# Optimization experiments

Measured on AMD Instinct MI355X. Metric: run time of the kernel, lower is better.

The kernel has to match this reference:

```python
import jax, jax.numpy as jnp
import numpy as np

N = 100000   # nodes
E = 1600000  # edges (self-loop free by construction)
B = 512      # graphs in batch
F = 128      # input node features
HID = 128    # hidden dim
HEADS = 4
CH = HID // HEADS  # 32
EPS_BN = 1e-5


def setup_inputs() -> dict:
    key = jax.random.key(0)
    ks = jax.random.split(key, 24)
    x = jax.random.normal(ks[0], (N, F), jnp.float32)
    dst = jax.random.randint(ks[1], (E,), 0, N)
    off = jax.random.randint(ks[2], (E,), 1, N)
    src = (dst + off) % N  # guaranteed no self loops
    edge_index = jnp.stack([src, dst]).astype(jnp.int32)
    batch = jnp.sort(jax.random.randint(ks[3], (N,), 0, B)).astype(jnp.int32)
    g = lambda k, shape, fan: jax.random.normal(k, shape, jnp.float32) / np.sqrt(fan)
    return {
        "x": x, "edge_index": edge_index, "batch": batch,
        "W_in": g(ks[4], (F, HID), F), "b_in": jnp.zeros((HID,), jnp.float32),
        "lin_w": g(ks[5], (2, HID, HID), HID),
        "att_src": g(ks[6], (2, HEADS, CH), CH),
        "att_dst": g(ks[7], (2, HEADS, CH), CH),
        "conv_b": jnp.zeros((2, HID), jnp.float32),
        "lin_w_last": g(ks[8], (HID, HID), HID),
        "att_src_last": g(ks[9], (HID,), HID),
        "att_dst_last": g(ks[10], (HID,), HID),
        "b_last": jnp.zeros((HID,), jnp.float32),
        "bn_g": jnp.ones((3, HID), jnp.float32) + 0.1 * jax.random.normal(ks[11], (3, HID), jnp.float32),
        "bn_b": 0.1 * jax.random.normal(ks[12], (3, HID), jnp.float32),
        "bn_m": 0.1 * jax.random.normal(ks[13], (3, HID), jnp.float32),
        "bn_v": 0.5 + jax.random.uniform(ks[14], (3, HID), jnp.float32),
        "ro_w1": g(ks[15], (HID, HID // 2), HID),
        "ro_b1": jnp.zeros((HID // 2,), jnp.float32),
        "ro_w2": g(ks[16], (HID // 2, 1), HID // 2),
        "ro_b2": jnp.zeros((1,), jnp.float32),
    }


def _gat_conv(h, src, dst, W, a_src, a_dst, bias, concat):
    """PyG GATConv (shared lin for src/dst, add_self_loops=True, eval mode)."""
    n = h.shape[0]
    heads, ch = a_src.shape
    xs = (h @ W).reshape(n, heads, ch)              # [N,H,C]
    al_s = jnp.sum(xs * a_src, axis=-1)             # [N,H]
    al_d = jnp.sum(xs * a_dst, axis=-1)             # [N,H]
    loop = jnp.arange(n, dtype=src.dtype)
    src_f = jnp.concatenate([src, loop])
    dst_f = jnp.concatenate([dst, loop])
    e = jax.nn.leaky_relu(al_s[src_f] + al_d[dst_f], 0.2)   # [E+N,H]
    m = jax.ops.segment_max(e, dst_f, num_segments=n)       # dest-grouped softmax
    ee = jnp.exp(e - m[dst_f])
    z = jax.ops.segment_sum(ee, dst_f, num_segments=n)
    alpha = ee / (z[dst_f] + 1e-16)                          # [E+N,H]
    out = jax.ops.segment_sum(alpha[:, :, None] * xs[src_f], dst_f, num_segments=n)
    out = out.reshape(n, heads * ch) if concat else jnp.mean(out, axis=1)
    return out + bias


def _bn_eval(h, g, b, m, v):
    return (h - m) * (g / jnp.sqrt(v + EPS_BN)) + b


def _seg_softmax(scores, seg, num_segments):
    m = jax.ops.segment_max(scores, seg, num_segments=num_segments)
    e = jnp.exp(scores - m[seg])
    z = jax.ops.segment_sum(e, seg, num_segments=num_segments)
    return e / z[seg]


def reference(x, edge_index, batch, W_in, b_in, lin_w, att_src, att_dst, conv_b,
              lin_w_last, att_src_last, att_dst_last, b_last,
              bn_g, bn_b, bn_m, bn_v, ro_w1, ro_b1, ro_w2, ro_b2):
    src, dst = edge_index[0], edge_index[1]
    h = x @ W_in + b_in                                       # input_proj
    # first num_layers-1 multi-head concat layers
    for i in range(2):
        h_new = _gat_conv(h, src, dst, lin_w[i], att_src[i], att_dst[i], conv_b[i], True)
        h_new = jax.nn.elu(_bn_eval(h_new, bn_g[i], bn_b[i], bn_m[i], bn_v[i]))
        h = h + h_new                                         # residual (shapes match)
    # final single-head layer, concat=False
    h_new = _gat_conv(h, src, dst, lin_w_last, att_src_last[None, :], att_dst_last[None, :], b_last, False)
    h_new = jax.nn.elu(_bn_eval(h_new, bn_g[2], bn_b[2], bn_m[2], bn_v[2]))
    h = h + h_new
    # attention readout + per-graph softmax over atoms
    atom_scores = (jnp.tanh(h @ ro_w1 + ro_b1) @ ro_w2 + ro_b2)[:, 0]   # [N]
    atom_attention = _seg_softmax(atom_scores, batch, B)
    # attention-weighted add pool
    graph_emb = jax.ops.segment_sum(h * atom_attention[:, None], batch, num_segments=B)
    return graph_emb, atom_attention
```

## Files before the change

kernel.cpp:

```cpp
#include <hip/hip_runtime.h>
#include <math.h>
#include <stdint.h>

#define BSZ 512
#define BSH 9
#define NBKT_MAX 256

typedef __attribute__((ext_vector_type(8))) short bf16x8;
typedef __attribute__((ext_vector_type(4))) float f32x4;

static __device__ __forceinline__ uint32_t f2bf(float x) {
    uint32_t u = __float_as_uint(x);
    return (u + 0x7fffu + ((u >> 16) & 1u)) >> 16;
}
static __device__ __forceinline__ float bflo(uint32_t v) { return __uint_as_float(v << 16); }
static __device__ __forceinline__ float bfhi(uint32_t v) { return __uint_as_float(v & 0xffff0000u); }
static __device__ __forceinline__ void split2(float x, short& hi, short& lo) {
    uint32_t hb = f2bf(x);
    float hf = __uint_as_float(hb << 16);
    uint32_t lb = f2bf(x - hf);
    hi = (short)hb; lo = (short)lb;
}

__global__ void k_binit(int* __restrict__ bcur, int nbkt, int cap) {
    int t = threadIdx.x;
    if (t < nbkt) bcur[t] = t * cap;
}
__global__ __launch_bounds__(256) void k_bucket(const int* __restrict__ src, const int* __restrict__ dst,
                                                int* __restrict__ bcur, uint32_t* __restrict__ bucketed,
                                                int e, int cap) {
    __shared__ int hist[NBKT_MAX];
    __shared__ int cur[NBKT_MAX];
    int t = threadIdx.x;
    hist[t] = 0;
    __syncthreads();
    int base = blockIdx.x * 8192;
#pragma unroll 4
    for (int i = 0; i < 32; ++i) {
        int ei = base + i * 256 + t;
        if (ei < e) atomicAdd(&hist[dst[ei] >> BSH], 1);
    }
    __syncthreads();
    int hc = hist[t];
    cur[t] = (hc > 0) ? atomicAdd(&bcur[t], hc) : 0;
    __syncthreads();
#pragma unroll 4
    for (int i = 0; i < 32; ++i) {
        int ei = base + i * 256 + t;
        if (ei < e) {
            int d = dst[ei], s = src[ei];
            int b = d >> BSH;
            int p = atomicAdd(&cur[b], 1);
            if (p < (b + 1) * cap)
                bucketed[p] = ((uint32_t)(d & (BSZ - 1)) << 23) | (uint32_t)s;
        }
    }
}
__global__ __launch_bounds__(256) void k_bcount(const int* __restrict__ bcur, const uint32_t* __restrict__ bucketed,
                                                int* __restrict__ cnt, int n, int cap) {
    __shared__ int lf[BSZ];
    int b = blockIdx.x, t = threadIdx.x;
    int n0 = b << BSH;
    int nn = min(BSZ, n - n0);
    for (int i = t; i < nn; i += 256) lf[i] = 0;
    __syncthreads();
    int cb = min(bcur[b] - b * cap, cap);
    const uint32_t* ba = bucketed + (size_t)b * cap;
    for (int i = t; i < cb; i += 256) atomicAdd(&lf[ba[i] >> 23], 1);
    __syncthreads();
    for (int i = t; i < nn; i += 256) cnt[n0 + i] = lf[i] + 1;
}
__global__ __launch_bounds__(256) void k_scan1(const int* __restrict__ cnt, int* __restrict__ bsum, int n) {
    __shared__ int sd[256];
    int base = blockIdx.x * 1024, t = threadIdx.x;
    int s = 0;
#pragma unroll
    for (int i = 0; i < 4; ++i) {
        int idx = base + t * 4 + i;
        if (idx < n) s += (cnt[idx] + 3) & ~3;
    }
    sd[t] = s; __syncthreads();
    for (int o = 128; o; o >>= 1) {
        if (t < o) sd[t] += sd[t + o];
        __syncthreads();
    }
    if (t == 0) bsum[blockIdx.x] = sd[0];
}
__global__ void k_scan2(int* __restrict__ bsum, int nb) {
    __shared__ int sd[128];
    int t = threadIdx.x;
    int v = (t < nb) ? bsum[t] : 0;
    sd[t] = v; __syncthreads();
    for (int o = 1; o < 128; o <<= 1) {
        int u = (t >= o) ? sd[t - o] : 0;
        __syncthreads();
        sd[t] += u;
        __syncthreads();
    }
    if (t < nb) bsum[t] = sd[t] - v;
}
__global__ __launch_bounds__(256) void k_scan3(const int* __restrict__ cnt, const int* __restrict__ bsum,
                                               int* __restrict__ rp, int n) {
    __shared__ int sd[256];
    int base = blockIdx.x * 1024, t = threadIdx.x;
    int v[4]; int s = 0;
#pragma unroll
    for (int i = 0; i < 4; ++i) {
        int idx = base + t * 4 + i;
        v[i] = (idx < n) ? ((cnt[idx] + 3) & ~3) : 0;
        s += v[i];
    }
    sd[t] = s; __syncthreads();
    for (int o = 1; o < 256; o <<= 1) {
        int u = (t >= o) ? sd[t - o] : 0;
        __syncthreads();
        sd[t] += u;
        __syncthreads();
    }
    int excl = sd[t] - s + bsum[blockIdx.x];
#pragma unroll
    for (int i = 0; i < 4; ++i) {
        int idx = base + t * 4 + i;
        if (idx < n) rp[idx] = excl;
        excl += v[i];
        if (idx == n - 1) rp[n] = excl;
    }
}
__global__ __launch_bounds__(256) void k_bscatter(const int* __restrict__ bcur, const uint32_t* __restrict__ bucketed,
                                                  const int* __restrict__ rp, int* __restrict__ col,
                                                  int n, int cap) {
    __shared__ int lf[BSZ];
    __shared__ int rpl[BSZ];
    int b = blockIdx.x, t = threadIdx.x;
    int n0 = b << BSH;
    int nn = min(BSZ, n - n0);
    for (int i = t; i < nn; i += 256) {
        int r = rp[n0 + i];
        rpl[i] = r;
        lf[i] = 1;
        col[r] = n0 + i;
    }
    __syncthreads();
    int cb = min(bcur[b] - b * cap, cap);
    const uint32_t* ba = bucketed + (size_t)b * cap;
    for (int i = t; i < cb; i += 256) {
        uint32_t v = ba[i];
        int ld = (int)(v >> 23), s = (int)(v & 0x7fffffu);
        int o = atomicAdd(&lf[ld], 1);
        col[rpl[ld] + o] = s;
    }
    __syncthreads();
    for (int i = t; i < nn; i += 256) {
        int c = lf[i], end = (c + 3) & ~3;
        int r = rpl[i];
        for (int j = c; j < end; ++j) col[r + j] = -1;
    }
}
__global__ void k_bnprep(const float* __restrict__ conv_b, const float* __restrict__ b_last,
                         const float* __restrict__ bn_g, const float* __restrict__ bn_b,
                         const float* __restrict__ bn_m, const float* __restrict__ bn_v,
                         float* __restrict__ sc, float* __restrict__ sh) {
    int i = blockIdx.x * 128 + threadIdx.x;
    if (i >= 384) return;
    int layer = i >> 7, c = i & 127;
    float bias = (layer < 2) ? conv_b[layer * 128 + c] : b_last[c];
    float s = bn_g[i] * __frsqrt_rn(bn_v[i] + 1e-5f);
    sc[i] = s;
    sh[i] = (bias - bn_m[i]) * s + bn_b[i];
}
__global__ __launch_bounds__(256) void k_wprep(const float* __restrict__ W_in, const float* __restrict__ lin_w,
                                               const float* __restrict__ lin_w_last,
                                               uint16_t* __restrict__ wfh, uint16_t* __restrict__ wfl) {
    int i = blockIdx.x * 256 + threadIdx.x;
    int m = i >> 14, e = i & 16383;
    const float* src = (m == 0) ? W_in : (m == 1) ? lin_w : (m == 2) ? (lin_w + 16384) : lin_w_last;
    float v = src[e];
    int k = e >> 7, n = e & 127;
    int kc = k >> 5, g = (k >> 3) & 3, j = k & 7, ct = n >> 4, cln = n & 15;
    int idx = m * 16384 + (((kc * 8 + ct) * 64) + g * 16 + cln) * 8 + j;
    short hi, lo;
    split2(v, hi, lo);
    wfh[idx] = hi; wfl[idx] = lo;
}

template <int ATT, int OBF>
__global__ __launch_bounds__(256) void k_gemm(
    const float* __restrict__ A, const uint16_t* __restrict__ wfh, const uint16_t* __restrict__ wfl,
    const float* __restrict__ bias, void* __restrict__ outv,
    const float* __restrict__ atts, const float* __restrict__ attd,
    float* __restrict__ als, float* __restrict__ ald, int nrows)
{
    __shared__ __align__(16) uint16_t sbuf[4][16][144];
    const int t = threadIdx.x;
    const int l = t & 63, wv = t >> 6;
    const int cl = l & 15, gl = l >> 4;
    const int row0w = blockIdx.x * 128 + wv * 32;

    float bloc[8], avsl[8], avdl[8];
    if (ATT == 0) {
#pragma unroll
        for (int ct = 0; ct < 8; ++ct) bloc[ct] = bias[ct * 16 + cl];
    } else {
#pragma unroll
        for (int ct = 0; ct < 8; ++ct) { avsl[ct] = atts[ct * 16 + cl]; avdl[ct] = attd[ct * 16 + cl]; }
    }

    bf16x8 Ah[2][4], Al[2][4];
#pragma unroll
    for (int rt = 0; rt < 2; ++rt) {
        int row = row0w + rt * 16 + cl;
        bool ok = row < nrows;
        const float* ap = A + (size_t)row * 128 + gl * 8;
#pragma unroll
        for (int kc = 0; kc < 4; ++kc) {
            float4 u = make_float4(0.f, 0.f, 0.f, 0.f), v = u;
            if (ok) {
                u = *(const float4*)(ap + kc * 32);
                v = *(const float4*)(ap + kc * 32 + 4);
            }
            float xv[8] = {u.x, u.y, u.z, u.w, v.x, v.y, v.z, v.w};
            bf16x8 hbv, lbv;
#pragma unroll
            for (int j = 0; j < 8; ++j) {
                short hi, lo;
                split2(xv[j], hi, lo);
                hbv[j] = hi; lbv[j] = lo;
            }
            Ah[rt][kc] = hbv; Al[rt][kc] = lbv;
        }
    }

    f32x4 acc[2][8];
#pragma unroll
    for (int rt = 0; rt < 2; ++rt)
#pragma unroll
        for (int ct = 0; ct < 8; ++ct) { f32x4 z = {0.f, 0.f, 0.f, 0.f}; acc[rt][ct] = z; }
#pragma unroll
    for (int kc = 0; kc < 4; ++kc) {
        bf16x8 bh[8], bl[8];
#pragma unroll
        for (int ct = 0; ct < 8; ++ct) {
            bh[ct] = *(const bf16x8*)(wfh + (size_t)(((kc * 8 + ct) * 64) + l) * 8);
            bl[ct] = *(const bf16x8*)(wfl + (size_t)(((kc * 8 + ct) * 64) + l) * 8);
        }
#pragma unroll
        for (int rt = 0; rt < 2; ++rt)
#pragma unroll
            for (int ct = 0; ct < 8; ++ct) {
                acc[rt][ct] = __builtin_amdgcn_mfma_f32_16x16x32_bf16(Ah[rt][kc], bh[ct], acc[rt][ct], 0, 0, 0);
                acc[rt][ct] = __builtin_amdgcn_mfma_f32_16x16x32_bf16(Ah[rt][kc], bl[ct], acc[rt][ct], 0, 0, 0);
                acc[rt][ct] = __builtin_amdgcn_mfma_f32_16x16x32_bf16(Al[rt][kc], bh[ct], acc[rt][ct], 0, 0, 0);
            }
    }

    if (OBF) {
        uint16_t* out = (uint16_t*)outv;
        uint16_t* buf = &sbuf[wv][0][0];
#pragma unroll
        for (int rt = 0; rt < 2; ++rt) {
#pragma unroll
            for (int ct = 0; ct < 8; ++ct)
#pragma unroll
                for (int r = 0; r < 4; ++r)
                    buf[(gl * 4 + r) * 144 + ct * 16 + cl] = (uint16_t)f2bf(acc[rt][ct][r]);
#pragma unroll
            for (int ri = 0; ri < 4; ++ri) {
                int rloc = ri * 4 + gl;
                int row = row0w + rt * 16 + rloc;
                if (row < nrows) {
                    uint4 v = *(const uint4*)&buf[rloc * 144 + cl * 8];
                    *(uint4*)&out[(size_t)row * 128 + cl * 8] = v;
                }
            }
        }
    } else {
        float* out = (float*)outv;
#pragma unroll
        for (int rt = 0; rt < 2; ++rt)
#pragma unroll
            for (int r = 0; r < 4; ++r) {
                int row = row0w + rt * 16 + gl * 4 + r;
                if (row < nrows) {
#pragma unroll
                    for (int ct = 0; ct < 8; ++ct)
                        out[(size_t)row * 128 + ct * 16 + cl] = acc[rt][ct][r] + bloc[ct];
                }
            }
    }

    if (ATT == 4) {
#pragma unroll
        for (int rt = 0; rt < 2; ++rt)
#pragma unroll
            for (int r = 0; r < 4; ++r) {
                float s[4], d[4];
#pragma unroll
                for (int hh = 0; hh < 4; ++hh) {
                    s[hh] = acc[rt][2 * hh][r] * avsl[2 * hh] + acc[rt][2 * hh + 1][r] * avsl[2 * hh + 1];
                    d[hh] = acc[rt][2 * hh][r] * avdl[2 * hh] + acc[rt][2 * hh + 1][r] * avdl[2 * hh + 1];
                }
#pragma unroll
                for (int hh = 0; hh < 4; ++hh) {
                    s[hh] += __shfl_xor(s[hh], 1); s[hh] += __shfl_xor(s[hh], 2);
                    s[hh] += __shfl_xor(s[hh], 4); s[hh] += __shfl_xor(s[hh], 8);
                    d[hh] += __shfl_xor(d[hh], 1); d[hh] += __shfl_xor(d[hh], 2);
                    d[hh] += __shfl_xor(d[hh], 4); d[hh] += __shfl_xor(d[hh], 8);
                }
                int row = row0w + rt * 16 + gl * 4 + r;
                if (row < nrows && cl < 4) { als[row * 4 + cl] = s[cl]; ald[row * 4 + cl] = d[cl]; }
            }
    } else if (ATT == 1) {
#pragma unroll
        for (int rt = 0; rt < 2; ++rt)
#pragma unroll
            for (int r = 0; r < 4; ++r) {
                float s = 0.f, d = 0.f;
#pragma unroll
                for (int ct = 0; ct < 8; ++ct) {
                    s += acc[rt][ct][r] * avsl[ct];
                    d += acc[rt][ct][r] * avdl[ct];
                }
                s += __shfl_xor(s, 1); s += __shfl_xor(s, 2); s += __shfl_xor(s, 4); s += __shfl_xor(s, 8);
                d += __shfl_xor(d, 1); d += __shfl_xor(d, 2); d += __shfl_xor(d, 4); d += __shfl_xor(d, 8);
                int row = row0w + rt * 16 + gl * 4 + r;
                if (row < nrows && cl == 0) { als[row] = s; ald[row] = d; }
            }
    }
}

template <int H>
__global__ __launch_bounds__(256) void k_agg(
    const int* __restrict__ rp, const int* __restrict__ col,
    const float* __restrict__ als, const float* __restrict__ ald_,
    const uint16_t* __restrict__ xs, const float* __restrict__ bnsc,
    const float* __restrict__ bnsh, float* __restrict__ h, int n)
{
    constexpr int EPG = (H == 4) ? 16 : 64;
    int node = blockIdx.x * 4 + (threadIdx.x >> 6);
    if (node >= n) return;
    int l = threadIdx.x & 63;
    int hl = (H == 4) ? (l >> 4) : 0;
    int lbase = (H == 4) ? (l & 48) : 0;
    int c0 = l * 2;
    float ad = ald_[node * H + hl];
    int jb = rp[node], je = rp[node + 1];
    float2 hv = *(const float2*)&h[(size_t)node * 128 + c0];
    float sc0v = bnsc[c0], sc1v = bnsc[c0 + 1];
    float sh0v = bnsh[c0], sh1v = bnsh[c0 + 1];

    float z = 0.f, a0 = 0.f, a1 = 0.f;
    for (int j = jb; j < je; j += EPG) {
        int e_l = j + (l & (EPG - 1));
        int s_l = (e_l < je) ? col[e_l] : -1;
        int t_l = s_l < 0 ? 0 : s_l;
        float lg = ((H == 4) ? als[t_l * 4 + hl] : als[t_l]) + ad;
        lg = fmaxf(lg, 0.2f * lg);
        float p_l = (s_l < 0) ? 0.f : __expf(lg);
        int ng = min(EPG, je - j);
        int q = 0;
        for (; q + 8 <= ng; q += 8) {
            int4 ca = *(const int4*)&col[j + q];
            int4 cb = *(const int4*)&col[j + q + 4];
            float p0 = __shfl(p_l, lbase | (q + 0));
            float p1 = __shfl(p_l, lbase | (q + 1));
            float p2 = __shfl(p_l, lbase | (q + 2));
            float p3 = __shfl(p_l, lbase | (q + 3));
            float p4 = __shfl(p_l, lbase | (q + 4));
            float p5 = __shfl(p_l, lbase | (q + 5));
            float p6 = __shfl(p_l, lbase | (q + 6));
            float p7 = __shfl(p_l, lbase | (q + 7));
            int t0 = max(ca.x, 0), t1 = max(ca.y, 0), t2 = max(ca.z, 0), t3 = max(ca.w, 0);
            int t4 = max(cb.x, 0), t5 = max(cb.y, 0), t6 = max(cb.z, 0), t7 = max(cb.w, 0);
            uint32_t x0 = *(const uint32_t*)(xs + (size_t)t0 * 128 + c0);
            uint32_t x1 = *(const uint32_t*)(xs + (size_t)t1 * 128 + c0);
            uint32_t x2 = *(const uint32_t*)(xs + (size_t)t2 * 128 + c0);
            uint32_t x3 = *(const uint32_t*)(xs + (size_t)t3 * 128 + c0);
            uint32_t x4 = *(const uint32_t*)(xs + (size_t)t4 * 128 + c0);
            uint32_t x5 = *(const uint32_t*)(xs + (size_t)t5 * 128 + c0);
            uint32_t x6 = *(const uint32_t*)(xs + (size_t)t6 * 128 + c0);
            uint32_t x7 = *(const uint32_t*)(xs + (size_t)t7 * 128 + c0);
            z += ((p0 + p1) + (p2 + p3)) + ((p4 + p5) + (p6 + p7));
            float s0 = fmaf(p0, bflo(x0), fmaf(p1, bflo(x1), fmaf(p2, bflo(x2), p3 * bflo(x3))));
            float s1 = fmaf(p4, bflo(x4), fmaf(p5, bflo(x5), fmaf(p6, bflo(x6), p7 * bflo(x7))));
            a0 += s0 + s1;
            float u0 = fmaf(p0, bfhi(x0), fmaf(p1, bfhi(x1), fmaf(p2, bfhi(x2), p3 * bfhi(x3))));
            float u1 = fmaf(p4, bfhi(x4), fmaf(p5, bfhi(x5), fmaf(p6, bfhi(x6), p7 * bfhi(x7))));
            a1 += u0 + u1;
        }
        if (q < ng) {
            int4 ca = *(const int4*)&col[j + q];
            float p0 = __shfl(p_l, lbase | (q + 0));
            float p1 = __shfl(p_l, lbase | (q + 1));
            float p2 = __shfl(p_l, lbase | (q + 2));
            float p3 = __shfl(p_l, lbase | (q + 3));
            int t0 = max(ca.x, 0), t1 = max(ca.y, 0), t2 = max(ca.z, 0), t3 = max(ca.w, 0);
            uint32_t x0 = *(const uint32_t*)(xs + (size_t)t0 * 128 + c0);
            uint32_t x1 = *(const uint32_t*)(xs + (size_t)t1 * 128 + c0);
            uint32_t x2 = *(const uint32_t*)(xs + (size_t)t2 * 128 + c0);
            uint32_t x3 = *(const uint32_t*)(xs + (size_t)t3 * 128 + c0);
            z += (p0 + p1) + (p2 + p3);
            a0 = fmaf(p0, bflo(x0), fmaf(p1, bflo(x1), fmaf(p2, bflo(x2), fmaf(p3, bflo(x3), a0))));
            a1 = fmaf(p0, bfhi(x0), fmaf(p1, bfhi(x1), fmaf(p2, bfhi(x2), fmaf(p3, bfhi(x3), a1))));
        }
    }
    float inv = 1.f / z;
    float y0 = fmaf(a0 * inv, sc0v, sh0v);
    float y1 = fmaf(a1 * inv, sc1v, sh1v);
    y0 = y0 > 0.f ? y0 : expm1f(y0);
    y1 = y1 > 0.f ? y1 : expm1f(y1);
    hv.x += y0; hv.y += y1;
    *(float2*)&h[(size_t)node * 128 + c0] = hv;
}

__global__ __launch_bounds__(256) void k_scores(
    const float* __restrict__ h, const float* __restrict__ w1, const float* __restrict__ b1,
    const float* __restrict__ w2, const float* __restrict__ b2,
    float* __restrict__ scores, int n)
{
    __shared__ float W1s[128 * 64];
    __shared__ float As[16][132];
    __shared__ float red[4][32][4];
    const int t = threadIdx.x;
    {
        const float4* w4 = (const float4*)w1;
        float4* s4 = (float4*)W1s;
#pragma unroll
        for (int i = 0; i < 8; ++i) s4[t + i * 256] = w4[t + i * 256];
    }
    const int rg = t & 31, cg = t >> 5;
    const int r0 = rg * 4, c0 = cg * 8;
    const int row0 = blockIdx.x * 128;
    const int ar = (t * 2) >> 2;
    const int ak0 = ((t * 2) & 3) * 4, ak1 = ((t * 2 + 1) & 3) * 4;
    float bloc[8], w2loc[8];
#pragma unroll
    for (int j = 0; j < 8; ++j) { bloc[j] = b1[c0 + j]; w2loc[j] = w2[c0 + j]; }

    float acc[4][8] = {};
    for (int kc = 0; kc < 8; ++kc) {
        __syncthreads();
        {
            float4 v0 = make_float4(0.f, 0.f, 0.f, 0.f), v1 = v0;
            int row = row0 + ar;
            if (row < n) {
                v0 = *(const float4*)&h[(size_t)row * 128 + kc * 16 + ak0];
                v1 = *(const float4*)&h[(size_t)row * 128 + kc * 16 + ak1];
            }
            As[ak0 + 0][ar] = v0.x; As[ak0 + 1][ar] = v0.y; As[ak0 + 2][ar] = v0.z; As[ak0 + 3][ar] = v0.w;
            As[ak1 + 0][ar] = v1.x; As[ak1 + 1][ar] = v1.y; As[ak1 + 2][ar] = v1.z; As[ak1 + 3][ar] = v1.w;
        }
        __syncthreads();
#pragma unroll
        for (int kk = 0; kk < 16; ++kk) {
            float a[4], w[8];
            *(float4*)&a[0] = *(const float4*)&As[kk][r0];
            *(float4*)&w[0] = *(const float4*)&W1s[(kc * 16 + kk) * 64 + c0];
            *(float4*)&w[4] = *(const float4*)&W1s[(kc * 16 + kk) * 64 + c0 + 4];
#pragma unroll
            for (int r = 0; r < 4; ++r)
#pragma unroll
                for (int j = 0; j < 8; ++j) acc[r][j] += a[r] * w[j];
        }
    }
    float part[4];
#pragma unroll
    for (int r = 0; r < 4; ++r) {
        float s = 0.f;
#pragma unroll
        for (int j = 0; j < 8; ++j) s += tanhf(acc[r][j] + bloc[j]) * w2loc[j];
        part[r] = s;
    }
#pragma unroll
    for (int r = 0; r < 4; ++r) part[r] += __shfl_xor(part[r], 32);
    const int wv = t >> 6;
    if ((t & 32) == 0) {
#pragma unroll
        for (int r = 0; r < 4; ++r) red[wv][rg][r] = part[r];
    }
    __syncthreads();
    if (t < 128) {
        int row = row0 + t;
        if (row < n) {
            float s = red[0][t >> 2][t & 3] + red[1][t >> 2][t & 3]
                    + red[2][t >> 2][t & 3] + red[3][t >> 2][t & 3];
            scores[row] = s + b2[0];
        }
    }
}
__global__ void k_graph_ptr(const int* __restrict__ batch, int* __restrict__ gptr, int n, int B) {
    int i = blockIdx.x * 256 + threadIdx.x;
    if (i >= n) return;
    int b = batch[i];
    int bp = (i == 0) ? -1 : batch[i - 1];
    for (int g = bp + 1; g <= b; ++g) gptr[g] = i;
    if (i == n - 1)
        for (int g = b + 1; g <= B; ++g) gptr[g] = n;
}
__global__ __launch_bounds__(256) void k_graph_mz(const int* __restrict__ gptr, const float* __restrict__ scores,
                                                  float* __restrict__ gmax, float* __restrict__ gz, int B) {
    int g = blockIdx.x * 4 + (threadIdx.x >> 6);
    if (g >= B) return;
    int l = threadIdx.x & 63;
    int s0 = gptr[g], s1 = gptr[g + 1];
    float m = -INFINITY;
    for (int i = s0 + l; i < s1; i += 64) m = fmaxf(m, scores[i]);
#pragma unroll
    for (int off = 32; off; off >>= 1) m = fmaxf(m, __shfl_xor(m, off));
    float z = 0.f;
    for (int i = s0 + l; i < s1; i += 64) z += __expf(scores[i] - m);
#pragma unroll
    for (int off = 32; off; off >>= 1) z += __shfl_xor(z, off);
    if (l == 0) { gmax[g] = m; gz[g] = z; }
}
__global__ void k_att(const int* __restrict__ batch, const float* __restrict__ scores,
                      const float* __restrict__ gmax, const float* __restrict__ gz,
                      float* __restrict__ att, int n) {
    int i = blockIdx.x * 256 + threadIdx.x;
    if (i >= n) return;
    int b = batch[i];
    att[i] = __expf(scores[i] - gmax[b]) / gz[b];
}
__global__ __launch_bounds__(256) void k_emb(const int* __restrict__ gptr, const float* __restrict__ att,
                                             const float* __restrict__ h, float* __restrict__ emb) {
    __shared__ float sd[16][64];
    int g = blockIdx.x >> 1, half = blockIdx.x & 1;
    int t = threadIdx.x;
    int cq = (t & 15) * 4;
    int c = half * 64 + cq;
    int p = t >> 4;
    int s0 = gptr[g], s1 = gptr[g + 1];
    float4 acc = make_float4(0.f, 0.f, 0.f, 0.f);
    for (int i = s0 + p; i < s1; i += 16) {
        float a = att[i];
        float4 hvv = *(const float4*)&h[(size_t)i * 128 + c];
        acc.x += a * hvv.x; acc.y += a * hvv.y; acc.z += a * hvv.z; acc.w += a * hvv.w;
    }
    *(float4*)&sd[p][cq] = acc;
    __syncthreads();
    if (t < 64) {
        float s = 0.f;
#pragma unroll
        for (int q = 0; q < 16; ++q) s += sd[q][t];
        emb[g * 128 + half * 64 + t] = s;
    }
}

extern "C" void kernel_launch(void* const* d_in, const int* in_sizes, int n_in,
                              void* d_out, int out_size, void* d_ws, size_t ws_size,
                              hipStream_t stream)
{
    const float* x            = (const float*)d_in[0];
    const int*   eidx         = (const int*)d_in[1];
    const int*   batch        = (const int*)d_in[2];
    const float* W_in         = (const float*)d_in[3];
    const float* b_in         = (const float*)d_in[4];
    const float* lin_w        = (const float*)d_in[5];
    const float* att_src      = (const float*)d_in[6];
    const float* att_dst      = (const float*)d_in[7];
    const float* conv_b       = (const float*)d_in[8];
    const float* lin_w_last   = (const float*)d_in[9];
    const float* att_src_last = (const float*)d_in[10];
    const float* att_dst_last = (const float*)d_in[11];
    const float* b_last       = (const float*)d_in[12];
    const float* bn_g         = (const float*)d_in[13];
    const float* bn_b         = (const float*)d_in[14];
    const float* bn_m         = (const float*)d_in[15];
    const float* bn_v         = (const float*)d_in[16];
    const float* ro_w1        = (const float*)d_in[17];
    const float* ro_b1        = (const float*)d_in[18];
    const float* ro_w2        = (const float*)d_in[19];
    const float* ro_b2        = (const float*)d_in[20];

    const int N = in_sizes[0] / 128;
    const int E = in_sizes[1] / 2;
    const int B = 512;
    const int* esrc = eidx;
    const int* edst = eidx + E;
    const int colcap = E + 4 * N + 64;
    const int NBKT = (N + BSZ - 1) >> BSH;
    const int cap = (E / NBKT) * 3 / 2 + 512;

    char* wsp = (char*)d_ws;
    size_t off = 0;
    auto alloc = [&](size_t bytes) -> void* {
        void* p = wsp + off;
        off += (bytes + 511) & ~(size_t)511;
        return p;
    };
    float*    h      = (float*)alloc((size_t)N * 128 * 4);
    uint16_t* xs     = (uint16_t*)alloc((size_t)N * 128 * 2);
    float*    als    = (float*)alloc((size_t)N * 4 * 4);
    float*    ald    = (float*)alloc((size_t)N * 4 * 4);
    float*    scores = (float*)alloc((size_t)N * 4);
    int*      rp     = (int*)alloc((size_t)(N + 1) * 4);
    int*      col    = (int*)alloc((size_t)colcap * 4);
    int*      cnt    = (int*)alloc((size_t)N * 4);
    int*      bsum   = (int*)alloc(4096);
    int*      gptr   = (int*)alloc((size_t)(B + 1) * 4);
    float*    gmax   = (float*)alloc((size_t)B * 4);
    float*    gz     = (float*)alloc((size_t)B * 4);
    float*    bnsc   = (float*)alloc(384 * 4);
    float*    bnsh   = (float*)alloc(384 * 4);
    int*      bcur   = (int*)alloc(NBKT_MAX * 4);
    uint16_t* wfh    = (uint16_t*)alloc(4 * 16384 * 2);
    uint16_t* wfl    = (uint16_t*)alloc(4 * 16384 * 2);
    uint32_t* bucketed = (uint32_t*)alloc((size_t)NBKT * cap * 4);
    (void)ws_size; (void)n_in; (void)out_size;

    float* emb = (float*)d_out;
    float* att = (float*)d_out + (size_t)B * 128;

    const int nb = (N + 1023) / 1024;
    hipLaunchKernelGGL(k_binit, dim3(1), dim3(256), 0, stream, bcur, NBKT, cap);
    hipLaunchKernelGGL(k_bucket, dim3((E + 8191) / 8192), dim3(256), 0, stream,
                       esrc, edst, bcur, bucketed, E, cap);
    hipLaunchKernelGGL(k_bcount, dim3(NBKT), dim3(256), 0, stream, bcur, bucketed, cnt, N, cap);
    hipLaunchKernelGGL(k_scan1, dim3(nb), dim3(256), 0, stream, cnt, bsum, N);
    hipLaunchKernelGGL(k_scan2, dim3(1), dim3(128), 0, stream, bsum, nb);
    hipLaunchKernelGGL(k_scan3, dim3(nb), dim3(256), 0, stream, cnt, bsum, rp, N);
    hipLaunchKernelGGL(k_bscatter, dim3(NBKT), dim3(256), 0, stream, bcur, bucketed, rp, col, N, cap);
    hipLaunchKernelGGL(k_bnprep, dim3(3), dim3(128), 0, stream, conv_b, b_last, bn_g, bn_b, bn_m, bn_v, bnsc, bnsh);
    hipLaunchKernelGGL(k_wprep, dim3(256), dim3(256), 0, stream, W_in, lin_w, lin_w_last, wfh, wfl);

    const int ntiles = (N + 127) / 128;
    hipLaunchKernelGGL((k_gemm<0, 0>), dim3(ntiles), dim3(256), 0, stream,
                       x, wfh, wfl, b_in, (void*)h, (const float*)nullptr, (const float*)nullptr,
                       (float*)nullptr, (float*)nullptr, N);
    for (int i = 0; i < 2; ++i) {
        hipLaunchKernelGGL((k_gemm<4, 1>), dim3(ntiles), dim3(256), 0, stream,
                           h, wfh + (size_t)(i + 1) * 16384, wfl + (size_t)(i + 1) * 16384,
                           (const float*)nullptr, (void*)xs,
                           att_src + i * 128, att_dst + i * 128, als, ald, N);
        hipLaunchKernelGGL((k_agg<4>), dim3((N + 3) / 4), dim3(256), 0, stream,
                           rp, col, als, ald, xs, bnsc + i * 128, bnsh + i * 128, h, N);
    }
    hipLaunchKernelGGL((k_gemm<1, 1>), dim3(ntiles), dim3(256), 0, stream,
                       h, wfh + (size_t)3 * 16384, wfl + (size_t)3 * 16384,
                       (const float*)nullptr, (void*)xs,
                       att_src_last, att_dst_last, als, ald, N);
    hipLaunchKernelGGL((k_agg<1>), dim3((N + 3) / 4), dim3(256), 0, stream,
                       rp, col, als, ald, xs, bnsc + 256, bnsh + 256, h, N);

    hipLaunchKernelGGL(k_scores, dim3(ntiles), dim3(256), 0, stream,
                       h, ro_w1, ro_b1, ro_w2, ro_b2, scores, N);
    hipLaunchKernelGGL(k_graph_ptr, dim3((N + 255) / 256), dim3(256), 0, stream, batch, gptr, N, B);
    hipLaunchKernelGGL(k_graph_mz, dim3((B + 3) / 4), dim3(256), 0, stream, gptr, scores, gmax, gz, B);
    hipLaunchKernelGGL(k_att, dim3((N + 255) / 256), dim3(256), 0, stream, batch, scores, gmax, gz, att, N);
    hipLaunchKernelGGL(k_emb, dim3(B * 2), dim3(256), 0, stream, gptr, att, h, emb);
}
```

Baseline: 497.7 us.

## Stage fp32 GEMM output through LDS and use ds_swizzle broadcasts in aggregation

The fp32 GEMM epilogue now writes accumulators to a padded shared-memory tile and emits coalesced float4 row stores, replacing strided scalar stores. In the 4-head aggregation kernel, per-edge weight broadcasts use ds_swizzle within 16-lane groups instead of generic shuffles. Edge groups are dispatched on their exact size (16/12/8/4), which assumes CSR rows are padded to multiples of 4. The softmax denominator is now accumulated per lane and reduced once with xor-shuffles at the end, removing the per-edge sums.

```diff
diff --git a/kernel.cpp b/kernel.cpp
--- a/kernel.cpp
+++ b/kernel.cpp
@@ -190,7 +190,7 @@
     const float* __restrict__ atts, const float* __restrict__ attd,
     float* __restrict__ als, float* __restrict__ ald, int nrows)
 {
-    __shared__ __align__(16) uint16_t sbuf[4][16][144];
+    __shared__ __align__(16) char smem[4 * 16 * 132 * 4];
     const int t = threadIdx.x;
     const int l = t & 63, wv = t >> 6;
     const int cl = l & 15, gl = l >> 4;
@@ -255,7 +255,7 @@
 
     if (OBF) {
         uint16_t* out = (uint16_t*)outv;
-        uint16_t* buf = &sbuf[wv][0][0];
+        uint16_t* buf = (uint16_t*)smem + wv * (16 * 144);
 #pragma unroll
         for (int rt = 0; rt < 2; ++rt) {
 #pragma unroll
@@ -275,17 +275,26 @@
         }
     } else {
         float* out = (float*)outv;
-#pragma unroll
-        for (int rt = 0; rt < 2; ++rt)
-#pragma unroll
-            for (int r = 0; r < 4; ++r) {
-                int row = row0w + rt * 16 + gl * 4 + r;
+        float* buf = (float*)smem + wv * (16 * 132);
+#pragma unroll
+        for (int rt = 0; rt < 2; ++rt) {
+#pragma unroll
+            for (int ct = 0; ct < 8; ++ct)
+#pragma unroll
+                for (int r = 0; r < 4; ++r)
+                    buf[(gl * 4 + r) * 132 + ct * 16 + cl] = acc[rt][ct][r] + bloc[ct];
+#pragma unroll
+            for (int ri = 0; ri < 4; ++ri) {
+                int rloc = ri * 4 + gl;
+                int row = row0w + rt * 16 + rloc;
                 if (row < nrows) {
-#pragma unroll
-                    for (int ct = 0; ct < 8; ++ct)
-                        out[(size_t)row * 128 + ct * 16 + cl] = acc[rt][ct][r] + bloc[ct];
+                    float4 v0 = *(const float4*)&buf[rloc * 132 + cl * 8];
+                    float4 v1 = *(const float4*)&buf[rloc * 132 + cl * 8 + 4];
+                    *(float4*)&out[(size_t)row * 128 + cl * 8] = v0;
+                    *(float4*)&out[(size_t)row * 128 + cl * 8 + 4] = v1;
                 }
             }
+        }
     }
 
     if (ATT == 4) {
@@ -327,6 +336,31 @@
             }
     }
 }
+
+#define BC4(q) __int_as_float(__builtin_amdgcn_ds_swizzle(pi, 0x10 | ((q) << 5)))
+#define GATH(i, u) uint32_t x##i = *(const uint32_t*)(xsb + ((size_t)(u) << 7));
+#define EDGE8_H4(Q) do { \
+    int4 ca = *(const int4*)&col[j + (Q)]; \
+    int4 cb = *(const int4*)&col[j + (Q) + 4]; \
+    float p0 = BC4((Q)+0), p1 = BC4((Q)+1), p2 = BC4((Q)+2), p3 = BC4((Q)+3); \
+    float p4 = BC4((Q)+4), p5 = BC4((Q)+5), p6 = BC4((Q)+6), p7 = BC4((Q)+7); \
+    int u0 = max(ca.x, 0), u1 = max(ca.y, 0), u2 = max(ca.z, 0), u3 = max(ca.w, 0); \
+    int u4 = max(cb.x, 0), u5 = max(cb.y, 0), u6 = max(cb.z, 0), u7 = max(cb.w, 0); \
+    GATH(0, u0) GATH(1, u1) GATH(2, u2) GATH(3, u3) \
+    GATH(4, u4) GATH(5, u5) GATH(6, u6) GATH(7, u7) \
+    a0 = fmaf(p0, bflo(x0), fmaf(p1, bflo(x1), fmaf(p2, bflo(x2), fmaf(p3, bflo(x3), a0)))); \
+    a0 = fmaf(p4, bflo(x4), fmaf(p5, bflo(x5), fmaf(p6, bflo(x6), fmaf(p7, bflo(x7), a0)))); \
+    a1 = fmaf(p0, bfhi(x0), fmaf(p1, bfhi(x1), fmaf(p2, bfhi(x2), fmaf(p3, bfhi(x3), a1)))); \
+    a1 = fmaf(p4, bfhi(x4), fmaf(p5, bfhi(x5), fmaf(p6, bfhi(x6), fmaf(p7, bfhi(x7), a1)))); \
+} while (0)
+#define EDGE4_H4(Q) do { \
+    int4 ca = *(const int4*)&col[j + (Q)]; \
+    float p0 = BC4((Q)+0), p1 = BC4((Q)+1), p2 = BC4((Q)+2), p3 = BC4((Q)+3); \
+    int u0 = max(ca.x, 0), u1 = max(ca.y, 0), u2 = max(ca.z, 0), u3 = max(ca.w, 0); \
+    GATH(0, u0) GATH(1, u1) GATH(2, u2) GATH(3, u3) \
+    a0 = fmaf(p0, bflo(x0), fmaf(p1, bflo(x1), fmaf(p2, bflo(x2), fmaf(p3, bflo(x3), a0)))); \
+    a1 = fmaf(p0, bfhi(x0), fmaf(p1, bfhi(x1), fmaf(p2, bfhi(x2), fmaf(p3, bfhi(x3), a1)))); \
+} while (0)
 
 template <int H>
 __global__ __launch_bounds__(256) void k_agg(
@@ -340,70 +374,65 @@
     if (node >= n) return;
     int l = threadIdx.x & 63;
     int hl = (H == 4) ? (l >> 4) : 0;
-    int lbase = (H == 4) ? (l & 48) : 0;
     int c0 = l * 2;
     float ad = ald_[node * H + hl];
     int jb = rp[node], je = rp[node + 1];
     float2 hv = *(const float2*)&h[(size_t)node * 128 + c0];
     float sc0v = bnsc[c0], sc1v = bnsc[c0 + 1];
     float sh0v = bnsh[c0], sh1v = bnsh[c0 + 1];
-
-    float z = 0.f, a0 = 0.f, a1 = 0.f;
+    const uint16_t* xsb = xs + c0;
+
+    float zl = 0.f, a0 = 0.f, a1 = 0.f;
     for (int j = jb; j < je; j += EPG) {
         int e_l = j + (l & (EPG - 1));
         int s_l = (e_l < je) ? col[e_l] : -1;
-        int t_l = s_l < 0 ? 0 : s_l;
+        int t_l = max(s_l, 0);
         float lg = ((H == 4) ? als[t_l * 4 + hl] : als[t_l]) + ad;
         lg = fmaxf(lg, 0.2f * lg);
         float p_l = (s_l < 0) ? 0.f : __expf(lg);
+        zl += p_l;
+        int pi = __float_as_int(p_l);
         int ng = min(EPG, je - j);
-        int q = 0;
-        for (; q + 8 <= ng; q += 8) {
-            int4 ca = *(const int4*)&col[j + q];
-            int4 cb = *(const int4*)&col[j + q + 4];
-            float p0 = __shfl(p_l, lbase | (q + 0));
-            float p1 = __shfl(p_l, lbase | (q + 1));
-            float p2 = __shfl(p_l, lbase | (q + 2));
-            float p3 = __shfl(p_l, lbase | (q + 3));
-            float p4 = __shfl(p_l, lbase | (q + 4));
-            float p5 = __shfl(p_l, lbase | (q + 5));
-            float p6 = __shfl(p_l, lbase | (q + 6));
-            float p7 = __shfl(p_l, lbase | (q + 7));
-            int t0 = max(ca.x, 0), t1 = max(ca.y, 0), t2 = max(ca.z, 0), t3 = max(ca.w, 0);
-            int t4 = max(cb.x, 0), t5 = max(cb.y, 0), t6 = max(cb.z, 0), t7 = max(cb.w, 0);
-            uint32_t x0 = *(const uint32_t*)(xs + (size_t)t0 * 128 + c0);
-            uint32_t x1 = *(const uint32_t*)(xs + (size_t)t1 * 128 + c0);
-            uint32_t x2 = *(const uint32_t*)(xs + (size_t)t2 * 128 + c0);
-            uint32_t x3 = *(const uint32_t*)(xs + (size_t)t3 * 128 + c0);
-            uint32_t x4 = *(const uint32_t*)(xs + (size_t)t4 * 128 + c0);
-            uint32_t x5 = *(const uint32_t*)(xs + (size_t)t5 * 128 + c0);
-            uint32_t x6 = *(const uint32_t*)(xs + (size_t)t6 * 128 + c0);
-            uint32_t x7 = *(const uint32_t*)(xs + (size_t)t7 * 128 + c0);
-            z += ((p0 + p1) + (p2 + p3)) + ((p4 + p5) + (p6 + p7));
-            float s0 = fmaf(p0, bflo(x0), fmaf(p1, bflo(x1), fmaf(p2, bflo(x2), p3 * bflo(x3))));
-            float s1 = fmaf(p4, bflo(x4), fmaf(p5, bflo(x5), fmaf(p6, bflo(x6), p7 * bflo(x7))));
-            a0 += s0 + s1;
-            float u0 = fmaf(p0, bfhi(x0), fmaf(p1, bfhi(x1), fmaf(p2, bfhi(x2), p3 * bfhi(x3))));
-            float u1 = fmaf(p4, bfhi(x4), fmaf(p5, bfhi(x5), fmaf(p6, bfhi(x6), p7 * bfhi(x7))));
-            a1 += u0 + u1;
-        }
-        if (q < ng) {
-            int4 ca = *(const int4*)&col[j + q];
-            float p0 = __shfl(p_l, lbase | (q + 0));
-            float p1 = __shfl(p_l, lbase | (q + 1));
-            float p2 = __shfl(p_l, lbase | (q + 2));
-            float p3 = __shfl(p_l, lbase | (q + 3));
-            int t0 = max(ca.x, 0), t1 = max(ca.y, 0), t2 = max(ca.z, 0), t3 = max(ca.w, 0);
-            uint32_t x0 = *(const uint32_t*)(xs + (size_t)t0 * 128 + c0);
-            uint32_t x1 = *(const uint32_t*)(xs + (size_t)t1 * 128 + c0);
-            uint32_t x2 = *(const uint32_t*)(xs + (size_t)t2 * 128 + c0);
-            uint32_t x3 = *(const uint32_t*)(xs + (size_t)t3 * 128 + c0);
-            z += (p0 + p1) + (p2 + p3);
-            a0 = fmaf(p0, bflo(x0), fmaf(p1, bflo(x1), fmaf(p2, bflo(x2), fmaf(p3, bflo(x3), a0))));
-            a1 = fmaf(p0, bfhi(x0), fmaf(p1, bfhi(x1), fmaf(p2, bfhi(x2), fmaf(p3, bfhi(x3), a1))));
-        }
-    }
-    float inv = 1.f / z;
+        if (H == 4) {
+            if (ng == 16)      { EDGE8_H4(0); EDGE8_H4(8); }
+            else if (ng == 12) { EDGE8_H4(0); EDGE4_H4(8); }
+            else if (ng == 8)  { EDGE8_H4(0); }
+            else               { EDGE4_H4(0); }
+        } else {
+            int q = 0;
+            for (; q + 8 <= ng; q += 8) {
+                int4 ca = *(const int4*)&col[j + q];
+                int4 cb = *(const int4*)&col[j + q + 4];
+                float p0 = __shfl(p_l, q + 0), p1 = __shfl(p_l, q + 1);
+                float p2 = __shfl(p_l, q + 2), p3 = __shfl(p_l, q + 3);
+                float p4 = __shfl(p_l, q + 4), p5 = __shfl(p_l, q + 5);
+                float p6 = __shfl(p_l, q + 6), p7 = __shfl(p_l, q + 7);
+                int u0 = max(ca.x, 0), u1 = max(ca.y, 0), u2 = max(ca.z, 0), u3 = max(ca.w, 0);
+                int u4 = max(cb.x, 0), u5 = max(cb.y, 0), u6 = max(cb.z, 0), u7 = max(cb.w, 0);
+                GATH(0, u0) GATH(1, u1) GATH(2, u2) GATH(3, u3)
+                GATH(4, u4) GATH(5, u5) GATH(6, u6) GATH(7, u7)
+                a0 = fmaf(p0, bflo(x0), fmaf(p1, bflo(x1), fmaf(p2, bflo(x2), fmaf(p3, bflo(x3), a0))));
+                a0 = fmaf(p4, bflo(x4), fmaf(p5, bflo(x5), fmaf(p6, bflo(x6), fmaf(p7, bflo(x7), a0))));
+                a1 = fmaf(p0, bfhi(x0), fmaf(p1, bfhi(x1), fmaf(p2, bfhi(x2), fmaf(p3, bfhi(x3), a1))));
+                a1 = fmaf(p4, bfhi(x4), fmaf(p5, bfhi(x5), fmaf(p6, bfhi(x6), fmaf(p7, bfhi(x7), a1))));
+            }
+            if (q < ng) {
+                int4 ca = *(const int4*)&col[j + q];
+                float p0 = __shfl(p_l, q + 0), p1 = __shfl(p_l, q + 1);
+                float p2 = __shfl(p_l, q + 2), p3 = __shfl(p_l, q + 3);
+                int u0 = max(ca.x, 0), u1 = max(ca.y, 0), u2 = max(ca.z, 0), u3 = max(ca.w, 0);
+                GATH(0, u0) GATH(1, u1) GATH(2, u2) GATH(3, u3)
+                a0 = fmaf(p0, bflo(x0), fmaf(p1, bflo(x1), fmaf(p2, bflo(x2), fmaf(p3, bflo(x3), a0))));
+                a1 = fmaf(p0, bfhi(x0), fmaf(p1, bfhi(x1), fmaf(p2, bfhi(x2), fmaf(p3, bfhi(x3), a1))));
+            }
+        }
+    }
+    zl += __shfl_xor(zl, 1); zl += __shfl_xor(zl, 2);
+    zl += __shfl_xor(zl, 4); zl += __shfl_xor(zl, 8);
+    if (H == 1) {
+        zl += __shfl_xor(zl, 16); zl += __shfl_xor(zl, 32);
+    }
+    float inv = 1.f / zl;
     float y0 = fmaf(a0 * inv, sc0v, sh0v);
     float y1 = fmaf(a1 * inv, sc1v, sh1v);
     y0 = y0 > 0.f ? y0 : expm1f(y0);
```

Result: no change. 501.7 us (+0.8%).

## Stage GEMM weights in LDS and stage fp32 output through shared memory

Applied to the files above, without the earlier changes.

The GEMM kernel now copies the split bf16 hi/lo weight fragments (64KB total) into shared memory at block start, and the MFMA loop reads B operands from LDS instead of global memory. The fp32 output path now also goes through a per-wave LDS buffer so each thread writes 16-byte vectors instead of scattered scalar stores, and the bf16 buffer row stride changes. This is meant to cut repeated global and L2 weight traffic and to coalesce the output writes. In exchange, 64KB of LDS per block lowers occupancy and adds two block-wide barriers.

```diff
diff --git a/kernel.cpp b/kernel.cpp
--- a/kernel.cpp
+++ b/kernel.cpp
@@ -190,11 +190,23 @@
     const float* __restrict__ atts, const float* __restrict__ attd,
     float* __restrict__ als, float* __restrict__ ald, int nrows)
 {
-    __shared__ __align__(16) uint16_t sbuf[4][16][144];
+    __shared__ __align__(16) char smem[65536];
     const int t = threadIdx.x;
     const int l = t & 63, wv = t >> 6;
     const int cl = l & 15, gl = l >> 4;
     const int row0w = blockIdx.x * 128 + wv * 32;
+
+    {
+        const uint4* gh = (const uint4*)wfh;
+        const uint4* glo = (const uint4*)wfl;
+        uint4* sh = (uint4*)smem;
+        uint4* sl = (uint4*)(smem + 32768);
+#pragma unroll
+        for (int i = 0; i < 8; ++i) {
+            sh[t + i * 256] = gh[t + i * 256];
+            sl[t + i * 256] = glo[t + i * 256];
+        }
+    }
 
     float bloc[8], avsl[8], avdl[8];
     if (ATT == 0) {
@@ -229,7 +241,10 @@
             Ah[rt][kc] = hbv; Al[rt][kc] = lbv;
         }
     }
-
+    __syncthreads();
+
+    const uint16_t* WH = (const uint16_t*)smem;
+    const uint16_t* WL = (const uint16_t*)(smem + 32768);
     f32x4 acc[2][8];
 #pragma unroll
     for (int rt = 0; rt < 2; ++rt)
@@ -240,8 +255,8 @@
         bf16x8 bh[8], bl[8];
 #pragma unroll
         for (int ct = 0; ct < 8; ++ct) {
-            bh[ct] = *(const bf16x8*)(wfh + (size_t)(((kc * 8 + ct) * 64) + l) * 8);
-            bl[ct] = *(const bf16x8*)(wfl + (size_t)(((kc * 8 + ct) * 64) + l) * 8);
+            bh[ct] = *(const bf16x8*)&WH[(((kc * 8 + ct) * 64) + l) * 8];
+            bl[ct] = *(const bf16x8*)&WL[(((kc * 8 + ct) * 64) + l) * 8];
         }
 #pragma unroll
         for (int rt = 0; rt < 2; ++rt)
@@ -252,40 +267,50 @@
                 acc[rt][ct] = __builtin_amdgcn_mfma_f32_16x16x32_bf16(Al[rt][kc], bh[ct], acc[rt][ct], 0, 0, 0);
             }
     }
+    __syncthreads();
 
     if (OBF) {
         uint16_t* out = (uint16_t*)outv;
-        uint16_t* buf = &sbuf[wv][0][0];
+        uint16_t* buf = (uint16_t*)(smem + wv * 16384);
 #pragma unroll
         for (int rt = 0; rt < 2; ++rt) {
 #pragma unroll
             for (int ct = 0; ct < 8; ++ct)
 #pragma unroll
                 for (int r = 0; r < 4; ++r)
-                    buf[(gl * 4 + r) * 144 + ct * 16 + cl] = (uint16_t)f2bf(acc[rt][ct][r]);
+                    buf[(gl * 4 + r) * 152 + ct * 16 + cl] = (uint16_t)f2bf(acc[rt][ct][r]);
 #pragma unroll
             for (int ri = 0; ri < 4; ++ri) {
                 int rloc = ri * 4 + gl;
                 int row = row0w + rt * 16 + rloc;
                 if (row < nrows) {
-                    uint4 v = *(const uint4*)&buf[rloc * 144 + cl * 8];
+                    uint4 v = *(const uint4*)&buf[rloc * 152 + cl * 8];
                     *(uint4*)&out[(size_t)row * 128 + cl * 8] = v;
                 }
             }
         }
     } else {
         float* out = (float*)outv;
-#pragma unroll
-        for (int rt = 0; rt < 2; ++rt)
-#pragma unroll
-            for (int r = 0; r < 4; ++r) {
-                int row = row0w + rt * 16 + gl * 4 + r;
+        float* buf = (float*)(smem + wv * 16384);
+#pragma unroll
+        for (int rt = 0; rt < 2; ++rt) {
+#pragma unroll
+            for (int ct = 0; ct < 8; ++ct)
+#pragma unroll
+                for (int r = 0; r < 4; ++r)
+                    buf[(gl * 4 + r) * 136 + ct * 16 + cl] = acc[rt][ct][r] + bloc[ct];
+#pragma unroll
+            for (int ri = 0; ri < 4; ++ri) {
+                int rloc = ri * 4 + gl;
+                int row = row0w + rt * 16 + rloc;
                 if (row < nrows) {
-#pragma unroll
-                    for (int ct = 0; ct < 8; ++ct)
-                        out[(size_t)row * 128 + ct * 16 + cl] = acc[rt][ct][r] + bloc[ct];
+                    float4 v0 = *(const float4*)&buf[rloc * 136 + cl * 8];
+                    float4 v1 = *(const float4*)&buf[rloc * 136 + cl * 8 + 4];
+                    *(float4*)&out[(size_t)row * 128 + cl * 8] = v0;
+                    *(float4*)&out[(size_t)row * 128 + cl * 8 + 4] = v1;
                 }
             }
+        }
     }
 
     if (ATT == 4) {
```

New measurement: 491.9 us. No clear change (-1.2%).
